# Performance work log

Measured on AMD Instinct MI355X. Metric: run time of the kernel, lower is better.

## Reference

```python
import jax, jax.numpy as jnp
import numpy as np

NUM_HEADS = 8
HEAD_DIM = 128
MAX_RES = 224.0


def rope_embed(feat_shape, dim, max_res=MAX_RES):
    # timm pixel_freq_bands: 2**linspace(0, log2(max_res)-1, dim//4) * pi
    num_bands = dim // 4
    bands = (2.0 ** jnp.linspace(0.0, float(np.log2(max_res)) - 1.0, num_bands)) * jnp.pi
    # pixel coords in [-1, 1] per spatial dim
    coords = [jnp.linspace(-1.0, 1.0, s) for s in feat_shape]
    grid = jnp.stack(jnp.meshgrid(*coords, indexing='ij'), axis=-1)[..., None]  # [H,W,2,1]
    pos = grid * bands  # [H,W,2,num_bands]
    n = int(np.prod(feat_shape))
    sin = jnp.repeat(jnp.sin(pos).reshape(n, -1), 2, axis=-1)  # [n, dim]
    cos = jnp.repeat(jnp.cos(pos).reshape(n, -1), 2, axis=-1)  # [n, dim]
    return sin, cos


def _rot(x):
    # interleaved rotate-half: (x0,x1,x2,x3,...) -> (-x1,x0,-x3,x2,...)
    return jnp.stack([-x[..., 1::2], x[..., ::2]], axis=-1).reshape(x.shape)


def setup_inputs() -> dict:
    key = jax.random.key(0)
    k1, k2, k3, k4 = jax.random.split(key, 4)
    C, E = 1024, 1024
    x = jax.random.normal(k1, (64, C, 16, 16), dtype=jnp.float32)
    qkv_w = jax.random.normal(k2, (3 * E, C), dtype=jnp.float32) * (C ** -0.5)
    qkv_b = jnp.zeros((3 * E,), dtype=jnp.float32)
    proj_w = jax.random.normal(k3, (E, E), dtype=jnp.float32) * (E ** -0.5)
    proj_b = jax.random.normal(k4, (E,), dtype=jnp.float32) * 0.02
    return {"x": x, "qkv_w": qkv_w, "qkv_b": qkv_b, "proj_w": proj_w, "proj_b": proj_b}


def reference(x, qkv_w, qkv_b, proj_w, proj_b):
    B, C, H, W = x.shape
    n = H * W
    scale = HEAD_DIM ** -0.5
    sin_emb, cos_emb = rope_embed((H, W), HEAD_DIM)  # [n, head_dim]

    t = x.reshape(B, C, n).transpose(0, 2, 1)                      # [B, n, C]
    t = jnp.concatenate([t.mean(axis=1, keepdims=True), t], axis=1)  # [B, n+1, C]

    qkv = t @ qkv_w.T + qkv_b                                      # [B, n+1, 3E]
    qkv = qkv.reshape(B, n + 1, 3, NUM_HEADS, HEAD_DIM).transpose(2, 0, 3, 1, 4)
    q, k, v = qkv[0], qkv[1], qkv[2]                               # [B, h, n+1, d]

    def apply_rope(z):
        zc, zs = z[:, :, :1], z[:, :, 1:]
        zs = zs * cos_emb + _rot(zs) * sin_emb
        return jnp.concatenate([zc, zs], axis=2)

    q = apply_rope(q)
    k = apply_rope(k)

    attn = jax.nn.softmax(jnp.einsum('bhqd,bhkd->bhqk', q, k) * scale, axis=-1)
    out = jnp.einsum('bhqk,bhkd->bhqd', attn, v)
    out = out.transpose(0, 2, 1, 3).reshape(B, n + 1, -1)           # [B, n+1, E]
    out = out @ proj_w.T + proj_b
    return out[:, 0]
```

## Files before the change

### kernel.cpp

```cpp
#include <hip/hip_runtime.h>
#include <math.h>

#define PI_F 3.14159265358979323846f
#define KSTEP 0.21959209425992272f

using bf16x8 = __attribute__((ext_vector_type(8))) short;
using f32x4 = __attribute__((ext_vector_type(4))) float;
using u16x8 = __attribute__((ext_vector_type(8))) unsigned short;

static __device__ __forceinline__ float wave_reduce_sum(float v) {
#pragma unroll
  for (int off = 32; off; off >>= 1) v += __shfl_down(v, off);
  return v;
}

static __device__ __forceinline__ unsigned short f2bf(float f) {
  unsigned u = __float_as_uint(f);
  return (unsigned short)((u + 0x7fffu + ((u >> 16) & 1u)) >> 16);
}

static __device__ __forceinline__ float bf2f(unsigned short s) {
  return __uint_as_float(((unsigned)s) << 16);
}

static __device__ __forceinline__ void gload_lds16(const void* g, void* l) {
  __builtin_amdgcn_global_load_lds((const __attribute__((address_space(1))) unsigned int*)g,
                                   (__attribute__((address_space(3))) unsigned int*)l, 16, 0, 0);
}

__global__ __launch_bounds__(256) void prep_kernel(const float* __restrict__ x,
                                                   const float* __restrict__ qkv_w,
                                                   const float* __restrict__ qkv_b,
                                                   unsigned short* __restrict__ xt,
                                                   float* __restrict__ t_mean,
                                                   unsigned short* __restrict__ wkT,
                                                   float2* __restrict__ sc) {
  const int bid = blockIdx.x;
  const int t = threadIdx.x;
  __shared__ float tile[64 * 33];
  __shared__ float tl2[64 * 65];
  if (bid < 1024) {
    const int ct = bid & 15, b = bid >> 4;
    const int cl = t >> 2, pq = (t & 3) * 8;
    const int pl = t >> 3, cq = (t & 7) * 8;
    float sum = 0.0f;
    const float* xrow = x + ((size_t)(b * 1024 + ct * 64 + cl) * 256) + pq;
    unsigned short* xtb = xt + (size_t)b * 262144 + ct * 64;
    for (int pt = 0; pt < 8; ++pt) {
      const float4 v0 = *reinterpret_cast<const float4*>(xrow + pt * 32);
      const float4 v1 = *reinterpret_cast<const float4*>(xrow + pt * 32 + 4);
      tile[cl * 33 + pq + 0] = v0.x; tile[cl * 33 + pq + 1] = v0.y;
      tile[cl * 33 + pq + 2] = v0.z; tile[cl * 33 + pq + 3] = v0.w;
      tile[cl * 33 + pq + 4] = v1.x; tile[cl * 33 + pq + 5] = v1.y;
      tile[cl * 33 + pq + 6] = v1.z; tile[cl * 33 + pq + 7] = v1.w;
      sum += (v0.x + v0.y) + (v0.z + v0.w) + (v1.x + v1.y) + (v1.z + v1.w);
      __syncthreads();
      u16x8 o;
#pragma unroll
      for (int e = 0; e < 8; ++e) o[e] = f2bf(tile[(cq + e) * 33 + pl]);
      *reinterpret_cast<u16x8*>(xtb + (size_t)(pt * 32 + pl) * 1024 + cq) = o;
      __syncthreads();
    }
    sum += __shfl_xor(sum, 1);
    sum += __shfl_xor(sum, 2);
    if ((t & 3) == 0) t_mean[b * 1024 + ct * 64 + cl] = sum * (1.0f / 256.0f);
  } else if (bid < 1280) {
    const int bb = bid - 1024;
    const int h = bb >> 5, t5 = bb & 31;
    const int dt = t5 >> 4, ct = t5 & 15;
    {
      const int dl = t >> 2, cq = (t & 3) * 16;
      const float* src = qkv_w + (size_t)(1024 + h * 128 + dt * 64 + dl) * 1024 + ct * 64 + cq;
#pragma unroll
      for (int i = 0; i < 4; ++i) {
        const float4 v = *reinterpret_cast<const float4*>(src + i * 4);
        tl2[dl * 65 + cq + i * 4 + 0] = v.x; tl2[dl * 65 + cq + i * 4 + 1] = v.y;
        tl2[dl * 65 + cq + i * 4 + 2] = v.z; tl2[dl * 65 + cq + i * 4 + 3] = v.w;
      }
    }
    __syncthreads();
    {
      const int cl = t >> 2, dq = (t & 3) * 16;
      unsigned short* dst = wkT + (size_t)(h * 1152 + ct * 64 + cl) * 128 + dt * 64 + dq;
      u16x8 o0, o1;
#pragma unroll
      for (int e = 0; e < 8; ++e) {
        o0[e] = f2bf(tl2[(dq + e) * 65 + cl]);
        o1[e] = f2bf(tl2[(dq + 8 + e) * 65 + cl]);
      }
      *reinterpret_cast<u16x8*>(dst) = o0;
      *reinterpret_cast<u16x8*>(dst + 8) = o1;
    }
  } else {
    const int idx = (bid - 1280) * 256 + t;
    const int m = idx >> 8, j = idx & 255;
    const float band = exp2f((float)(m & 31) * KSTEP) * PI_F;
    const float coord = (m < 32) ? (-1.0f + (2.0f / 15.0f) * (float)(j >> 4))
                                 : (-1.0f + (2.0f / 15.0f) * (float)(j & 15));
    float sn, cs;
    sincosf(coord * band, &sn, &cs);
    sc[idx] = make_float2(sn, cs);
  }
}

__global__ __launch_bounds__(256) void gemm_splitk(
    const float* __restrict__ A, int lda, int aStrideZ,
    const float* __restrict__ B, int ldb, int bStrideZ,
    float* __restrict__ Cp, int ldc, int cStrideZ, int cStrideKc, int KC) {
  const int nt = blockIdx.x, mt = blockIdx.y;
  const int z = blockIdx.z / KC, kc = blockIdx.z % KC;
  const int tid = threadIdx.x;
  A += (size_t)z * aStrideZ + (size_t)mt * 32 * lda + kc * 256;
  B += (size_t)z * bStrideZ + (size_t)nt * 64 * ldb + kc * 256;
  Cp += (size_t)kc * cStrideKc + (size_t)z * cStrideZ + (size_t)mt * 32 * ldc + nt * 64;

  __shared__ float As[32][34];
  __shared__ float Bs[32][68];

  const int tm = tid >> 4;
  const int tn = tid & 15;
  float acc0[4] = {0, 0, 0, 0}, acc1[4] = {0, 0, 0, 0};

  for (int k0 = 0; k0 < 256; k0 += 32) {
    {
      const int m = tid >> 3, kq = tid & 7;
      float4 v = *reinterpret_cast<const float4*>(A + (size_t)m * lda + k0 + kq * 4);
      As[kq * 4 + 0][m] = v.x; As[kq * 4 + 1][m] = v.y;
      As[kq * 4 + 2][m] = v.z; As[kq * 4 + 3][m] = v.w;
    }
#pragma unroll
    for (int r = 0; r < 2; ++r) {
      const int idx = r * 256 + tid;
      const int n = idx >> 3, kq = idx & 7;
      float4 v = *reinterpret_cast<const float4*>(B + (size_t)n * ldb + k0 + kq * 4);
      Bs[kq * 4 + 0][n] = v.x; Bs[kq * 4 + 1][n] = v.y;
      Bs[kq * 4 + 2][n] = v.z; Bs[kq * 4 + 3][n] = v.w;
    }
    __syncthreads();
#pragma unroll
    for (int k = 0; k < 32; ++k) {
      const float a0 = As[k][tm * 2], a1 = As[k][tm * 2 + 1];
      const float4 bb = *reinterpret_cast<const float4*>(&Bs[k][tn * 4]);
      acc0[0] += a0 * bb.x; acc0[1] += a0 * bb.y; acc0[2] += a0 * bb.z; acc0[3] += a0 * bb.w;
      acc1[0] += a1 * bb.x; acc1[1] += a1 * bb.y; acc1[2] += a1 * bb.z; acc1[3] += a1 * bb.w;
    }
    __syncthreads();
  }
  *reinterpret_cast<float4*>(Cp + (size_t)(tm * 2) * ldc + tn * 4) =
      make_float4(acc0[0], acc0[1], acc0[2], acc0[3]);
  *reinterpret_cast<float4*>(Cp + (size_t)(tm * 2 + 1) * ldc + tn * 4) =
      make_float4(acc1[0], acc1[1], acc1[2], acc1[3]);
}

__global__ __launch_bounds__(256) void gemm_proj_splitk(
    const float* __restrict__ Apart, const float* __restrict__ abias,
    const float* __restrict__ B, float* __restrict__ Cp) {
  const int nt = blockIdx.x, mt = blockIdx.y, kc = blockIdx.z;
  const int tid = threadIdx.x;
  B += (size_t)nt * 64 * 1024 + kc * 256;
  Cp += (size_t)kc * 65536 + (size_t)mt * 32 * 1024 + nt * 64;

  __shared__ float As[32][34];
  __shared__ float Bs[32][68];

  const int tm = tid >> 4;
  const int tn = tid & 15;
  float acc0[4] = {0, 0, 0, 0}, acc1[4] = {0, 0, 0, 0};

  for (int k0 = 0; k0 < 256; k0 += 32) {
    {
      const int m = tid >> 3, kq = tid & 7;
      const int kg = kc * 256 + k0 + kq * 4;
      const float* Ab = Apart + (size_t)(mt * 32 + m) * 1024 + kg;
      float4 v = *reinterpret_cast<const float4*>(abias + kg);
#pragma unroll
      for (int r = 0; r < 4; ++r) {
        const float4 p = *reinterpret_cast<const float4*>(Ab + (size_t)r * 65536);
        v.x += p.x; v.y += p.y; v.z += p.z; v.w += p.w;
      }
      As[kq * 4 + 0][m] = v.x; As[kq * 4 + 1][m] = v.y;
      As[kq * 4 + 2][m] = v.z; As[kq * 4 + 3][m] = v.w;
    }
#pragma unroll
    for (int r = 0; r < 2; ++r) {
      const int idx = r * 256 + tid;
      const int n = idx >> 3, kq = idx & 7;
      float4 v = *reinterpret_cast<const float4*>(B + (size_t)n * 1024 + k0 + kq * 4);
      Bs[kq * 4 + 0][n] = v.x; Bs[kq * 4 + 1][n] = v.y;
      Bs[kq * 4 + 2][n] = v.z; Bs[kq * 4 + 3][n] = v.w;
    }
    __syncthreads();
#pragma unroll
    for (int k = 0; k < 32; ++k) {
      const float a0 = As[k][tm * 2], a1 = As[k][tm * 2 + 1];
      const float4 bb = *reinterpret_cast<const float4*>(&Bs[k][tn * 4]);
      acc0[0] += a0 * bb.x; acc0[1] += a0 * bb.y; acc0[2] += a0 * bb.z; acc0[3] += a0 * bb.w;
      acc1[0] += a1 * bb.x; acc1[1] += a1 * bb.y; acc1[2] += a1 * bb.z; acc1[3] += a1 * bb.w;
    }
    __syncthreads();
  }
  *reinterpret_cast<float4*>(Cp + (size_t)(tm * 2) * 1024 + tn * 4) =
      make_float4(acc0[0], acc0[1], acc0[2], acc0[3]);
  *reinterpret_cast<float4*>(Cp + (size_t)(tm * 2 + 1) * 1024 + tn * 4) =
      make_float4(acc1[0], acc1[1], acc1[2], acc1[3]);
}

__global__ __launch_bounds__(256) void reduce4_bias(const float* __restrict__ part,
                                                    const float* __restrict__ bias,
                                                    float* __restrict__ out) {
  const int i = blockIdx.x * 256 + threadIdx.x;
  out[i] = part[i] + part[i + 65536] + part[i + 131072] + part[i + 196608] + bias[i & 1023];
}

__global__ __launch_bounds__(512, 1) void scores_u(
    const unsigned short* __restrict__ wkT, const unsigned short* __restrict__ xt,
    const float* __restrict__ q0p, const float* __restrict__ qkv_b,
    const float2* __restrict__ sc, const float* __restrict__ t_mean,
    float* __restrict__ u) {
  const int l = blockIdx.x;
  const int b = ((l >> 5) << 3) | (l & 7);
  const int ht = (l >> 3) & 3;
  const int tid = threadIdx.x;
  const int w = tid >> 6, lane = tid & 63;
  const int rgrp = lane >> 4;

  const int hh_ = w >> 2, sgen = (w >> 1) & 1, ch = w & 1;
  const int kap = hh_ * 2 + sgen;

  __shared__ __align__(16) char smem[143872];
  float* persist = reinterpret_cast<float*>(smem + 139264);
  float* q0l = persist;
  float* k0l = persist + 256;
  float* biasg = persist + 512;
  float* ps = persist + 576;
  float* smax = persist + 580;
  float* ssum = persist + 588;
  float* attnl = persist + 596;
  char* Btile = smem + 131072;

  const unsigned short* xtb = xt + (size_t)b * 262144;

#define STAGE_A(buf, c0)                                                        \
  {                                                                             \
    char* Ab_ = smem + (buf)*32768;                                             \
    _Pragma("unroll") for (int i = 0; i < 4; ++i) {                             \
      const int row_ = w * 32 + i * 8 + (lane >> 3);                            \
      const int sl_ = ((lane & 7) ^ ((row_ >> 1) & 7)) * 8;                     \
      gload_lds16(xtb + (size_t)row_ * 1024 + (c0) + sl_,                       \
                  Ab_ + (w * 4 + i) * 1024);                                    \
    }                                                                           \
  }
#define STAGE_W(buf, c0)                                                        \
  {                                                                             \
    char* Wb_ = smem + 65536 + (buf)*32768;                                     \
    _Pragma("unroll") for (int i = 0; i < 4; ++i) {                             \
      const int r_ = w * 16 + i * 4 + (lane >> 4);                  \
      const int c_ = r_ & 63;                                                   \
      const int L_ = lane & 15;                                                 \
      const int so_ = (L_ >> 3) * 64 + ((L_ & 7) ^ ((c_ >> 1) & 7)) * 8;        \
      gload_lds16(wkT + ((size_t)(ht * 2 + (r_ >> 6)) * 1152 + (c0) + c_) * 128 \
                      + so_,                                                    \
                  Wb_ + (w * 16 + i * 4) * 256);                                \
    }                                                                           \
  }

  STAGE_A(0, 0);
  STAGE_W(0, 0);
  if (tid < 256) {
    const float* qp = q0p + (size_t)b * 2048 + ht * 256 + tid;
    q0l[tid] = qkv_b[ht * 256 + tid] + qp[0] + qp[131072] + qp[262144] + qp[393216];
    const float* kp = qp + 1024;
    k0l[tid] = qkv_b[1024 + ht * 256 + tid] + kp[0] + kp[131072] + kp[262144] + kp[393216];
  }
  __syncthreads();

  bf16x8 rq[2];
  {
    const int v = lane & 15;
    const int jrep = sgen ? v : v * 16;
#pragma unroll
    for (int kk = 0; kk < 2; ++kk) {
#pragma unroll
      for (int e = 0; e < 8; e += 2) {
        const int d = kk * 32 + rgrp * 8 + e;
        const int p = d >> 1;
        const float qe = q0l[hh_ * 128 + sgen * 64 + 2 * p];
        const float qo = q0l[hh_ * 128 + sgen * 64 + 2 * p + 1];
        const float2 tt = sc[(sgen * 32 + p) * 256 + jrep];
        rq[kk][e] = (short)f2bf(qe * tt.y + qo * tt.x);
        rq[kk][e + 1] = (short)f2bf(qo * tt.y - qe * tt.x);
      }
    }
  }

  f32x4 acc[2][4] = {};
  for (int t = 0; t < 16; ++t) {
    {
      const int src = (t + 1 > 15) ? 15 : (t + 1);
      STAGE_A((t + 1) & 1, src * 64);
      STAGE_W((t + 1) & 1, src * 64);
    }
    asm volatile("s_waitcnt vmcnt(8)" ::: "memory");
    __builtin_amdgcn_s_barrier();
    const char* Ab = smem + (t & 1) * 32768;
    const char* Wb = smem + 65536 + (t & 1) * 32768;
    {
      f32x4 accg[2] = {};
#pragma unroll
      for (int kk = 0; kk < 2; ++kk) {
#pragma unroll
        for (int mt = 0; mt < 2; ++mt) {
          const int c_ = ch * 32 + mt * 16 + (lane & 15);
          const int slot = sgen * 8 + (((kk * 4 + rgrp)) ^ ((c_ >> 1) & 7));
          const bf16x8 wf = *reinterpret_cast<const bf16x8*>(
              Wb + (hh_ * 64 + c_) * 256 + (slot << 4));
          accg[mt] = __builtin_amdgcn_mfma_f32_16x16x32_bf16(wf, rq[kk], accg[mt], 0, 0, 0);
        }
      }
#pragma unroll
      for (int mt = 0; mt < 2; ++mt) {
        const int cl = ch * 32 + mt * 16 + rgrp * 4;
        const int n = kap * 16 + (lane & 15);
        const unsigned u0 = (unsigned)f2bf(accg[mt][0]) | ((unsigned)f2bf(accg[mt][1]) << 16);
        const unsigned u1 = (unsigned)f2bf(accg[mt][2]) | ((unsigned)f2bf(accg[mt][3]) << 16);
        *reinterpret_cast<uint2*>(Btile + n * 128 + ((((cl >> 3) ^ ((n >> 1) & 7))) << 4) +
                                  (rgrp & 1) * 8) = make_uint2(u0, u1);
      }
    }
    asm volatile("s_waitcnt lgkmcnt(0)" ::: "memory");
    __builtin_amdgcn_s_barrier();
#pragma unroll
    for (int kk = 0; kk < 2; ++kk) {
      bf16x8 af[2], bfr[4];
#pragma unroll
      for (int mi = 0; mi < 2; ++mi) {
        const int row = w * 32 + mi * 16 + (lane & 15);
        const int slot = (kk * 4 + rgrp) ^ ((row >> 1) & 7);
        af[mi] = *reinterpret_cast<const bf16x8*>(Ab + row * 128 + (slot << 4));
      }
#pragma unroll
      for (int ni = 0; ni < 4; ++ni) {
        const int n = ni * 16 + (lane & 15);
        const int slot = (kk * 4 + rgrp) ^ ((n >> 1) & 7);
        bfr[ni] = *reinterpret_cast<const bf16x8*>(Btile + n * 128 + (slot << 4));
      }
      __builtin_amdgcn_s_setprio(1);
#pragma unroll
      for (int mi = 0; mi < 2; ++mi)
#pragma unroll
        for (int ni = 0; ni < 4; ++ni)
          acc[mi][ni] =
              __builtin_amdgcn_mfma_f32_16x16x32_bf16(af[mi], bfr[ni], acc[mi][ni], 0, 0, 0);
      __builtin_amdgcn_s_setprio(0);
    }
    __builtin_amdgcn_s_barrier();
    asm volatile("" ::: "memory");
  }
#undef STAGE_A
#undef STAGE_W

  asm volatile("s_waitcnt vmcnt(0)" ::: "memory");
  __syncthreads();

  float* Sp = reinterpret_cast<float*>(smem);
  float* upart = reinterpret_cast<float*>(smem + 16384);

#pragma unroll
  for (int mi = 0; mi < 2; ++mi)
#pragma unroll
    for (int ni = 0; ni < 4; ++ni)
#pragma unroll
      for (int rr = 0; rr < 4; ++rr) {
        const int j = w * 32 + mi * 16 + (rgrp << 2) + rr;
        const int col = ni * 16 + (lane & 15);
        const int s = (col >> 4) & 1;
        const int sel = s ? (j & 15) : (j >> 4);
        if ((col & 15) == sel) Sp[(j * 2 + (col >> 5)) * 2 + s] = acc[mi][ni][rr];
      }
  if (tid < 64) {
    const int h_ = tid >> 5, s_ = (tid >> 4) & 1, v_ = tid & 15;
    const float* bk = qkv_b + 1024 + (ht * 2 + h_) * 128 + s_ * 64;
    const int jrep = s_ ? v_ : v_ * 16;
    float a = 0.0f;
#pragma unroll 4
    for (int p = 0; p < 32; ++p) {
      const float qe = q0l[h_ * 128 + s_ * 64 + 2 * p];
      const float qo = q0l[h_ * 128 + s_ * 64 + 2 * p + 1];
      const float2 tt = sc[(s_ * 32 + p) * 256 + jrep];
      a += (qe * tt.y + qo * tt.x) * bk[2 * p] + (qo * tt.y - qe * tt.x) * bk[2 * p + 1];
    }
    biasg[tid] = a;
  }
  if (tid < 256) {
    float pr = q0l[tid] * k0l[tid];
    pr = wave_reduce_sum(pr);
    if (lane == 0) ps[w] = pr;
  }
  __syncthreads();

  const float scale = 0.08838834764831845f;
  float e0 = 0.0f, e1 = 0.0f, eb0 = 0.0f, eb1 = 0.0f;
  if (tid < 256) {
    const float va0 = scale * (Sp[tid * 4 + 0] + Sp[tid * 4 + 1] + biasg[tid >> 4] +
                               biasg[16 + (tid & 15)]);
    const float va1 = scale * (Sp[tid * 4 + 2] + Sp[tid * 4 + 3] + biasg[32 + (tid >> 4)] +
                               biasg[48 + (tid & 15)]);
    float vb0 = -3.0e38f, vb1 = -3.0e38f;
    if (tid == 0) {
      vb0 = scale * (ps[0] + ps[1]);
      vb1 = scale * (ps[2] + ps[3]);
    }
    float m0 = fmaxf(va0, vb0), m1 = fmaxf(va1, vb1);
#pragma unroll
    for (int off = 32; off; off >>= 1) {
      m0 = fmaxf(m0, __shfl_xor(m0, off));
      m1 = fmaxf(m1, __shfl_xor(m1, off));
    }
    if (lane == 0) { smax[w] = m0; smax[4 + w] = m1; }
  }
  __syncthreads();
  if (tid < 256) {
    const float g0 = fmaxf(fmaxf(smax[0], smax[1]), fmaxf(smax[2], smax[3]));
    const float g1 = fmaxf(fmaxf(smax[4], smax[5]), fmaxf(smax[6], smax[7]));
    const float va0 = scale * (Sp[tid * 4 + 0] + Sp[tid * 4 + 1] + biasg[tid >> 4] +
                               biasg[16 + (tid & 15)]);
    const float va1 = scale * (Sp[tid * 4 + 2] + Sp[tid * 4 + 3] + biasg[32 + (tid >> 4)] +
                               biasg[48 + (tid & 15)]);
    e0 = expf(va0 - g0);
    e1 = expf(va1 - g1);
    if (tid == 0) {
      eb0 = expf(scale * (ps[0] + ps[1]) - g0);
      eb1 = expf(scale * (ps[2] + ps[3]) - g1);
    }
    float s0 = e0 + eb0, s1 = e1 + eb1;
#pragma unroll
    for (int off = 32; off; off >>= 1) {
      s0 += __shfl_xor(s0, off);
      s1 += __shfl_xor(s1, off);
    }
    if (lane == 0) { ssum[w] = s0; ssum[4 + w] = s1; }
  }
  __syncthreads();
  if (tid < 256) {
    const float inv0 = 1.0f / (ssum[0] + ssum[1] + ssum[2] + ssum[3]);
    const float inv1 = 1.0f / (ssum[4] + ssum[5] + ssum[6] + ssum[7]);
    attnl[1 + tid] = e0 * inv0;
    attnl[257 + 1 + tid] = e1 * inv1;
    if (tid == 0) { attnl[0] = eb0 * inv0; attnl[257] = eb1 * inv1; }
  }
  __syncthreads();

  {
    float ua0[16] = {}, ua1[16] = {};
    const unsigned short* xr = xtb + (size_t)(w * 32) * 1024 + lane * 16;
    for (int jj = 0; jj < 32; ++jj) {
      const float a0 = attnl[1 + w * 32 + jj];
      const float a1 = attnl[257 + 1 + w * 32 + jj];
      const u16x8 v0 = *reinterpret_cast<const u16x8*>(xr + (size_t)jj * 1024);
      const u16x8 v1 = *reinterpret_cast<const u16x8*>(xr + (size_t)jj * 1024 + 8);
#pragma unroll
      for (int e = 0; e < 8; ++e) {
        const float f0 = bf2f((unsigned short)v0[e]);
        const float f1 = bf2f((unsigned short)v1[e]);
        ua0[e] += a0 * f0; ua0[8 + e] += a0 * f1;
        ua1[e] += a1 * f0; ua1[8 + e] += a1 * f1;
      }
    }
#pragma unroll
    for (int e = 0; e < 16; ++e) {
      upart[(w * 2 + 0) * 1024 + lane * 16 + e] = ua0[e];
      upart[(w * 2 + 1) * 1024 + lane * 16 + e] = ua1[e];
    }
  }
  __syncthreads();
#pragma unroll
  for (int r = 0; r < 4; ++r) {
    const int o = tid * 4 + r;
    const int h2 = o >> 10, c = o & 1023;
    float s = 0.0f;
#pragma unroll
    for (int ww = 0; ww < 8; ++ww) s += upart[(ww * 2 + h2) * 1024 + c];
    s += attnl[h2 * 257] * t_mean[b * 1024 + c];
    u[((size_t)b * 8 + ht * 2 + h2) * 1024 + c] = s;
  }
}

extern "C" void kernel_launch(void* const* d_in, const int* in_sizes, int n_in,
                              void* d_out, int out_size, void* d_ws, size_t ws_size,
                              hipStream_t stream) {
  const float* x = (const float*)d_in[0];
  const float* qkv_w = (const float*)d_in[1];
  const float* qkv_b = (const float*)d_in[2];
  const float* proj_w = (const float*)d_in[3];
  const float* proj_b = (const float*)d_in[4];
  float* out = (float*)d_out;

  float* ws = (float*)d_ws;
  float* t_mean = ws;
  float* q0k0_part = ws + 65536;
  float* u = ws + 589824;
  float* out0_part = ws + 1114112;
  float* out_part = ws + 1376256;
  float2* sc = (float2*)(ws + 1638400);
  unsigned short* wkT = (unsigned short*)(ws + 1671168);
  unsigned short* x_t = (unsigned short*)(ws + 11698176);

  prep_kernel<<<1344, 256, 0, stream>>>(x, qkv_w, qkv_b, x_t, t_mean, wkT, sc);

  gemm_splitk<<<dim3(32, 2, 4), 256, 0, stream>>>(t_mean, 1024, 0, qkv_w, 1024, 0,
                                                  q0k0_part, 2048, 0, 131072, 4);

  scores_u<<<256, 512, 0, stream>>>(wkT, x_t, q0k0_part, qkv_b, sc, t_mean, u);

  gemm_splitk<<<dim3(2, 2, 32), 256, 0, stream>>>(u, 8192, 1024,
                                                  qkv_w + (size_t)2048 * 1024, 1024, 131072,
                                                  out0_part, 1024, 128, 65536, 4);

  gemm_proj_splitk<<<dim3(16, 2, 4), 256, 0, stream>>>(out0_part, qkv_b + 2048, proj_w, out_part);

  reduce4_bias<<<256, 256, 0, stream>>>(out_part, proj_b, out);
}
```

Baseline: 95.71 us.

## Halve K-chunk in scores_u to shrink LDS and raise occupancy

The scores_u kernel's K-loop chunk is halved from 64 to 32 channels (32 iterations instead of 16), shrinking double-buffered A/W tiles and the Btile so shared memory drops from about 140KB to about 73KB. Launch bounds move from one block per CU to four, letting more blocks co-reside to hide latency. The wave-to-work mapping of the K-projection MFMAs is reworked, and the attention-weighted sum over x is restructured so each wave covers a quarter of the channels over 128 rows, with only two partials to reduce. In exchange it doubles the number of barriers and loop iterations, and the higher launch bound may constrain registers and cause spills.

Measured after the change: 101.3 us. 5.9% more time.

```diff
diff --git a/kernel.cpp b/kernel.cpp
--- a/kernel.cpp
+++ b/kernel.cpp
@@ -212,7 +212,7 @@
   out[i] = part[i] + part[i + 65536] + part[i + 131072] + part[i + 196608] + bias[i & 1023];
 }
 
-__global__ __launch_bounds__(512, 1) void scores_u(
+__global__ __launch_bounds__(512, 4) void scores_u(
     const unsigned short* __restrict__ wkT, const unsigned short* __restrict__ xt,
     const float* __restrict__ q0p, const float* __restrict__ qkv_b,
     const float2* __restrict__ sc, const float* __restrict__ t_mean,
@@ -224,11 +224,10 @@
   const int w = tid >> 6, lane = tid & 63;
   const int rgrp = lane >> 4;
 
-  const int hh_ = w >> 2, sgen = (w >> 1) & 1, ch = w & 1;
-  const int kap = hh_ * 2 + sgen;
-
-  __shared__ __align__(16) char smem[143872];
-  float* persist = reinterpret_cast<float*>(smem + 139264);
+  const int hh_ = (w & 3) >> 1, sgen = (w & 3) & 1, ctl = w >> 2;
+
+  __shared__ __align__(16) char smem[74240];
+  float* persist = reinterpret_cast<float*>(smem + 69632);
   float* q0l = persist;
   float* k0l = persist + 256;
   float* biasg = persist + 512;
@@ -236,31 +235,31 @@
   float* smax = persist + 580;
   float* ssum = persist + 588;
   float* attnl = persist + 596;
-  char* Btile = smem + 131072;
+  char* Btile = smem + 65536;
 
   const unsigned short* xtb = xt + (size_t)b * 262144;
 
 #define STAGE_A(buf, c0)                                                        \
   {                                                                             \
-    char* Ab_ = smem + (buf)*32768;                                             \
-    _Pragma("unroll") for (int i = 0; i < 4; ++i) {                             \
-      const int row_ = w * 32 + i * 8 + (lane >> 3);                            \
-      const int sl_ = ((lane & 7) ^ ((row_ >> 1) & 7)) * 8;                     \
+    char* Ab_ = smem + (buf)*16384;                                             \
+    _Pragma("unroll") for (int i = 0; i < 2; ++i) {                             \
+      const int row_ = w * 32 + i * 16 + (lane >> 2);                           \
+      const int sl_ = ((lane & 3) ^ ((row_ >> 1) & 3)) * 8;                     \
       gload_lds16(xtb + (size_t)row_ * 1024 + (c0) + sl_,                       \
-                  Ab_ + (w * 4 + i) * 1024);                                    \
+                  Ab_ + (w * 2 + i) * 1024);                                    \
     }                                                                           \
   }
 #define STAGE_W(buf, c0)                                                        \
   {                                                                             \
-    char* Wb_ = smem + 65536 + (buf)*32768;                                     \
-    _Pragma("unroll") for (int i = 0; i < 4; ++i) {                             \
-      const int r_ = w * 16 + i * 4 + (lane >> 4);                  \
-      const int c_ = r_ & 63;                                                   \
+    char* Wb_ = smem + 32768 + (buf)*16384;                                     \
+    _Pragma("unroll") for (int i = 0; i < 2; ++i) {                             \
+      const int r_ = (w * 2 + i) * 4 + rgrp;                        \
+      const int c_ = r_ & 31;                                                   \
       const int L_ = lane & 15;                                                 \
       const int so_ = (L_ >> 3) * 64 + ((L_ & 7) ^ ((c_ >> 1) & 7)) * 8;        \
-      gload_lds16(wkT + ((size_t)(ht * 2 + (r_ >> 6)) * 1152 + (c0) + c_) * 128 \
+      gload_lds16(wkT + ((size_t)(ht * 2 + (r_ >> 5)) * 1152 + (c0) + c_) * 128 \
                       + so_,                                                    \
-                  Wb_ + (w * 16 + i * 4) * 256);                                \
+                  Wb_ + (w * 2 + i) * 1024);                                    \
     }                                                                           \
   }
 
@@ -294,55 +293,48 @@
   }
 
   f32x4 acc[2][4] = {};
-  for (int t = 0; t < 16; ++t) {
-    {
-      const int src = (t + 1 > 15) ? 15 : (t + 1);
-      STAGE_A((t + 1) & 1, src * 64);
-      STAGE_W((t + 1) & 1, src * 64);
-    }
-    asm volatile("s_waitcnt vmcnt(8)" ::: "memory");
+  for (int t = 0; t < 32; ++t) {
+    {
+      const int src = (t + 1 > 31) ? 31 : (t + 1);
+      STAGE_A((t + 1) & 1, src * 32);
+      STAGE_W((t + 1) & 1, src * 32);
+    }
+    asm volatile("s_waitcnt vmcnt(4)" ::: "memory");
     __builtin_amdgcn_s_barrier();
-    const char* Ab = smem + (t & 1) * 32768;
-    const char* Wb = smem + 65536 + (t & 1) * 32768;
-    {
-      f32x4 accg[2] = {};
+    const char* Ab = smem + (t & 1) * 16384;
+    const char* Wb = smem + 32768 + (t & 1) * 16384;
+    {
+      f32x4 accg = {};
 #pragma unroll
       for (int kk = 0; kk < 2; ++kk) {
-#pragma unroll
-        for (int mt = 0; mt < 2; ++mt) {
-          const int c_ = ch * 32 + mt * 16 + (lane & 15);
-          const int slot = sgen * 8 + (((kk * 4 + rgrp)) ^ ((c_ >> 1) & 7));
-          const bf16x8 wf = *reinterpret_cast<const bf16x8*>(
-              Wb + (hh_ * 64 + c_) * 256 + (slot << 4));
-          accg[mt] = __builtin_amdgcn_mfma_f32_16x16x32_bf16(wf, rq[kk], accg[mt], 0, 0, 0);
-        }
-      }
-#pragma unroll
-      for (int mt = 0; mt < 2; ++mt) {
-        const int cl = ch * 32 + mt * 16 + rgrp * 4;
-        const int n = kap * 16 + (lane & 15);
-        const unsigned u0 = (unsigned)f2bf(accg[mt][0]) | ((unsigned)f2bf(accg[mt][1]) << 16);
-        const unsigned u1 = (unsigned)f2bf(accg[mt][2]) | ((unsigned)f2bf(accg[mt][3]) << 16);
-        *reinterpret_cast<uint2*>(Btile + n * 128 + ((((cl >> 3) ^ ((n >> 1) & 7))) << 4) +
-                                  (rgrp & 1) * 8) = make_uint2(u0, u1);
-      }
+        const int c_ = ctl * 16 + (lane & 15);
+        const int slot = sgen * 8 + ((kk * 4 + rgrp) ^ ((c_ >> 1) & 7));
+        const bf16x8 wf = *reinterpret_cast<const bf16x8*>(
+            Wb + (hh_ * 32 + c_) * 256 + (slot << 4));
+        accg = __builtin_amdgcn_mfma_f32_16x16x32_bf16(wf, rq[kk], accg, 0, 0, 0);
+      }
+      const int n = (w & 3) * 16 + (lane & 15);
+      const int cslot = ctl * 2 + (rgrp >> 1);
+      const unsigned u0 = (unsigned)f2bf(accg[0]) | ((unsigned)f2bf(accg[1]) << 16);
+      const unsigned u1 = (unsigned)f2bf(accg[2]) | ((unsigned)f2bf(accg[3]) << 16);
+      *reinterpret_cast<uint2*>(Btile + n * 64 + ((cslot ^ ((n >> 1) & 3)) << 4) +
+                                (rgrp & 1) * 8) = make_uint2(u0, u1);
     }
     asm volatile("s_waitcnt lgkmcnt(0)" ::: "memory");
     __builtin_amdgcn_s_barrier();
-#pragma unroll
-    for (int kk = 0; kk < 2; ++kk) {
+    {
       bf16x8 af[2], bfr[4];
 #pragma unroll
       for (int mi = 0; mi < 2; ++mi) {
         const int row = w * 32 + mi * 16 + (lane & 15);
-        const int slot = (kk * 4 + rgrp) ^ ((row >> 1) & 7);
-        af[mi] = *reinterpret_cast<const bf16x8*>(Ab + row * 128 + (slot << 4));
+        const int slot = rgrp ^ ((row >> 1) & 3);
+        af[mi] = *reinterpret_cast<const bf16x8*>(Ab + row * 64 + (slot << 4));
       }
 #pragma unroll
       for (int ni = 0; ni < 4; ++ni) {
         const int n = ni * 16 + (lane & 15);
-        const int slot = (kk * 4 + rgrp) ^ ((n >> 1) & 7);
-        bfr[ni] = *reinterpret_cast<const bf16x8*>(Btile + n * 128 + (slot << 4));
+        const int slot = rgrp ^ ((n >> 1) & 3);
+        bfr[ni] = *reinterpret_cast<const bf16x8*>(Btile + n * 64 + (slot << 4));
       }
       __builtin_amdgcn_s_setprio(1);
 #pragma unroll
@@ -363,7 +355,7 @@
   __syncthreads();
 
   float* Sp = reinterpret_cast<float*>(smem);
-  float* upart = reinterpret_cast<float*>(smem + 16384);
+  float* up2 = reinterpret_cast<float*>(smem + 16384);
 
 #pragma unroll
   for (int mi = 0; mi < 2; ++mi)
@@ -451,25 +443,26 @@
   __syncthreads();
 
   {
-    float ua0[16] = {}, ua1[16] = {};
-    const unsigned short* xr = xtb + (size_t)(w * 32) * 1024 + lane * 16;
-    for (int jj = 0; jj < 32; ++jj) {
-      const float a0 = attnl[1 + w * 32 + jj];
-      const float a1 = attnl[257 + 1 + w * 32 + jj];
-      const u16x8 v0 = *reinterpret_cast<const u16x8*>(xr + (size_t)jj * 1024);
-      const u16x8 v1 = *reinterpret_cast<const u16x8*>(xr + (size_t)jj * 1024 + 8);
-#pragma unroll
-      for (int e = 0; e < 8; ++e) {
-        const float f0 = bf2f((unsigned short)v0[e]);
-        const float f1 = bf2f((unsigned short)v1[e]);
-        ua0[e] += a0 * f0; ua0[8 + e] += a0 * f1;
-        ua1[e] += a1 * f0; ua1[8 + e] += a1 * f1;
-      }
-    }
-#pragma unroll
-    for (int e = 0; e < 16; ++e) {
-      upart[(w * 2 + 0) * 1024 + lane * 16 + e] = ua0[e];
-      upart[(w * 2 + 1) * 1024 + lane * 16 + e] = ua1[e];
+    const int jh = w >> 2, cq = w & 3;
+    const int c0 = cq * 256 + lane * 4;
+    float ua0[4] = {}, ua1[4] = {};
+    const unsigned short* xr = xtb + c0;
+    for (int jj = 0; jj < 128; ++jj) {
+      const int j = jh * 128 + jj;
+      const float a0 = attnl[1 + j];
+      const float a1 = attnl[258 + j];
+      const ushort4 v = *reinterpret_cast<const ushort4*>(xr + (size_t)j * 1024);
+      const float xs[4] = {bf2f(v.x), bf2f(v.y), bf2f(v.z), bf2f(v.w)};
+#pragma unroll
+      for (int e = 0; e < 4; ++e) {
+        ua0[e] += a0 * xs[e];
+        ua1[e] += a1 * xs[e];
+      }
+    }
+#pragma unroll
+    for (int e = 0; e < 4; ++e) {
+      up2[jh * 2048 + 0 * 1024 + c0 + e] = ua0[e];
+      up2[jh * 2048 + 1 * 1024 + c0 + e] = ua1[e];
     }
   }
   __syncthreads();
@@ -477,9 +470,7 @@
   for (int r = 0; r < 4; ++r) {
     const int o = tid * 4 + r;
     const int h2 = o >> 10, c = o & 1023;
-    float s = 0.0f;
-#pragma unroll
-    for (int ww = 0; ww < 8; ++ww) s += upart[(ww * 2 + h2) * 1024 + c];
+    float s = up2[h2 * 1024 + c] + up2[2048 + h2 * 1024 + c];
     s += attnl[h2 * 257] * t_mean[b * 1024 + c];
     u[((size_t)b * 8 + ht * 2 + h2) * 1024 + c] = s;
   }
```

## Stage weight tiles through registers and restructure the double-buffer barrier schedule

Applied to the files above, without the earlier changes.

Weight tiles are now loaded from global memory into registers early in each iteration and written to LDS after the main MFMA phase, instead of using direct global-to-LDS loads. Per-lane source and destination addresses are computed once before the loop. The redundant prefetch on the final iteration is skipped, and the loop-top barrier is dropped so the A-tile wait is merged into the mid-iteration barrier. The aim is to hide weight-load latency behind compute and cut barrier overhead, at the cost of more registers and extra LDS write instructions.

After: 98.88 us. 3.3% more time.

```diff
diff --git a/kernel.cpp b/kernel.cpp
--- a/kernel.cpp
+++ b/kernel.cpp
@@ -240,6 +240,35 @@
 
   const unsigned short* xtb = xt + (size_t)b * 262144;
 
+  const int L15 = lane & 15;
+  const unsigned short* wbase[4];
+  int wdst[4];
+#pragma unroll
+  for (int i = 0; i < 4; ++i) {
+    const int r_ = w * 16 + i * 4 + (lane >> 4);
+    const int c_ = r_ & 63;
+    const int so_ = (L15 >> 3) * 64 + ((L15 & 7) ^ ((c_ >> 1) & 7)) * 8;
+    wbase[i] = wkT + ((size_t)(ht * 2 + (r_ >> 6)) * 1152 + c_) * 128 + so_;
+    wdst[i] = (w * 16 + i * 4) * 256 + lane * 16;
+  }
+
+  uint4 wT0, wT1, wT2, wT3;
+
+#define ISSUE_W(c0)                                                             \
+  {                                                                             \
+    wT0 = *reinterpret_cast<const uint4*>(wbase[0] + (size_t)(c0)*128);         \
+    wT1 = *reinterpret_cast<const uint4*>(wbase[1] + (size_t)(c0)*128);         \
+    wT2 = *reinterpret_cast<const uint4*>(wbase[2] + (size_t)(c0)*128);         \
+    wT3 = *reinterpret_cast<const uint4*>(wbase[3] + (size_t)(c0)*128);         \
+  }
+#define WRITE_W(buf)                                                            \
+  {                                                                             \
+    char* Wb_ = smem + 65536 + (buf)*32768;                                     \
+    *reinterpret_cast<uint4*>(Wb_ + wdst[0]) = wT0;                             \
+    *reinterpret_cast<uint4*>(Wb_ + wdst[1]) = wT1;                             \
+    *reinterpret_cast<uint4*>(Wb_ + wdst[2]) = wT2;                             \
+    *reinterpret_cast<uint4*>(Wb_ + wdst[3]) = wT3;                             \
+  }
 #define STAGE_A(buf, c0)                                                        \
   {                                                                             \
     char* Ab_ = smem + (buf)*32768;                                             \
@@ -250,22 +279,9 @@
                   Ab_ + (w * 4 + i) * 1024);                                    \
     }                                                                           \
   }
-#define STAGE_W(buf, c0)                                                        \
-  {                                                                             \
-    char* Wb_ = smem + 65536 + (buf)*32768;                                     \
-    _Pragma("unroll") for (int i = 0; i < 4; ++i) {                             \
-      const int r_ = w * 16 + i * 4 + (lane >> 4);                  \
-      const int c_ = r_ & 63;                                                   \
-      const int L_ = lane & 15;                                                 \
-      const int so_ = (L_ >> 3) * 64 + ((L_ & 7) ^ ((c_ >> 1) & 7)) * 8;        \
-      gload_lds16(wkT + ((size_t)(ht * 2 + (r_ >> 6)) * 1152 + (c0) + c_) * 128 \
-                      + so_,                                                    \
-                  Wb_ + (w * 16 + i * 4) * 256);                                \
-    }                                                                           \
-  }
-
+
+  ISSUE_W(0);
   STAGE_A(0, 0);
-  STAGE_W(0, 0);
   if (tid < 256) {
     const float* qp = q0p + (size_t)b * 2048 + ht * 256 + tid;
     q0l[tid] = qkv_b[ht * 256 + tid] + qp[0] + qp[131072] + qp[262144] + qp[393216];
@@ -293,15 +309,16 @@
     }
   }
 
+  WRITE_W(0);
+  asm volatile("s_waitcnt lgkmcnt(0)" ::: "memory");
+  __builtin_amdgcn_s_barrier();
+
   f32x4 acc[2][4] = {};
   for (int t = 0; t < 16; ++t) {
-    {
-      const int src = (t + 1 > 15) ? 15 : (t + 1);
-      STAGE_A((t + 1) & 1, src * 64);
-      STAGE_W((t + 1) & 1, src * 64);
-    }
-    asm volatile("s_waitcnt vmcnt(8)" ::: "memory");
-    __builtin_amdgcn_s_barrier();
+    if (t < 15) {
+      ISSUE_W((t + 1) * 64);
+      STAGE_A((t + 1) & 1, (t + 1) * 64);
+    }
     const char* Ab = smem + (t & 1) * 32768;
     const char* Wb = smem + 65536 + (t & 1) * 32768;
     {
@@ -328,6 +345,7 @@
       }
     }
     asm volatile("s_waitcnt lgkmcnt(0)" ::: "memory");
+    asm volatile("s_waitcnt vmcnt(8)" ::: "memory");
     __builtin_amdgcn_s_barrier();
 #pragma unroll
     for (int kk = 0; kk < 2; ++kk) {
@@ -353,11 +371,14 @@
               __builtin_amdgcn_mfma_f32_16x16x32_bf16(af[mi], bfr[ni], acc[mi][ni], 0, 0, 0);
       __builtin_amdgcn_s_setprio(0);
     }
+    if (t < 15) WRITE_W((t + 1) & 1);
+    asm volatile("s_waitcnt lgkmcnt(0)" ::: "memory");
     __builtin_amdgcn_s_barrier();
     asm volatile("" ::: "memory");
   }
+#undef ISSUE_W
+#undef WRITE_W
 #undef STAGE_A
-#undef STAGE_W
 
   asm volatile("s_waitcnt vmcnt(0)" ::: "memory");
   __syncthreads();
```
